# Kernel tuning notes

Hardware: AMD Instinct MI355X
Metric: run time of the kernel (lower is better)

Reference implementation:

```python
import jax, jax.numpy as jnp
import numpy as np

B, T, D = 2, 2048, 1024
H = 4            # num_heads (== num_kv_heads, num_kv_groups = 1)
W = 512          # window_size
S = 64           # state_size
CK = D // H      # head_k_dim = 256
CV = D // H      # head_v_dim = 256
EPS = 1e-5
SCALE = 1.0


def setup_inputs() -> dict:
    key = jax.random.key(0)
    ks = jax.random.split(key, 8)
    def w(k, o, i):
        return jax.random.normal(k, (o, i), jnp.float32) * 0.02
    return {
        "hidden_states": jax.random.normal(ks[0], (B, T, D), jnp.float32),
        "w_norm": jnp.ones((D,), jnp.float32),   # shared RMSNorm weight (pre- and post-norm; module overwrites self.norm)
        "Wq": w(ks[1], D, D),
        "Wk": w(ks[2], D, D),
        "Wv": w(ks[3], D, D),
        "Ws": w(ks[4], D, D),
        "Wg": w(ks[5], H * S, D),
        "Wo": w(ks[6], D, D),
    }


def _rms(x, w):
    return x * jax.lax.rsqrt(jnp.mean(x * x, axis=-1, keepdims=True) + EPS) * w


def reference(hidden_states, w_norm, Wq, Wk, Wv, Ws, Wg, Wo):
    h = _rms(hidden_states, w_norm)                           # pre-norm (norm_first)
    proj = lambda x, Wm: jnp.einsum('btd,od->bto', x, Wm)
    heads = lambda x, c: x.reshape(B, T, H, c).transpose(0, 2, 1, 3)
    q = heads(proj(h, Wq), CK) * SCALE                        # [B,H,T,CK]
    k = heads(proj(h, Wk), CK)
    v = heads(proj(h, Wv), CV)
    s = heads(proj(h, Ws), CK)                                # state-key projection
    g = jax.nn.softmax(proj(h, Wg), axis=-1)                  # softmax over full H*S dim (as in module)
    g = heads(g, S)                                           # [B,H,T,S] gate over state slots

    # ---- compressed global state (causal cumulative g-weighted outer products) ----
    # state_K[t] = sum_{t'<=t} g[t']^T s[t'];  scores_state[t,s] = q[t] . state_K[t,s]
    causal = jnp.tril(jnp.ones((T, T), dtype=bool))
    A = jnp.einsum('bhtc,bhuc->bhtu', q, s)                   # q . s per pair
    A = jnp.where(causal, A, 0.0)
    sc_state = jnp.einsum('bhtu,bhus->bhts', A, g)            # [B,H,T,S]

    # ---- sliding-window local attention (blocked: each query block sees prev+cur key block) ----
    nb = T // W
    qb = q.reshape(B, H, nb, W, CK)
    kb = k.reshape(B, H, nb, W, CK)
    vb = v.reshape(B, H, nb, W, CV)
    kprev = jnp.concatenate([jnp.zeros_like(kb[:, :, :1]), kb[:, :, :-1]], axis=2)
    vprev = jnp.concatenate([jnp.zeros_like(vb[:, :, :1]), vb[:, :, :-1]], axis=2)
    k2 = jnp.concatenate([kprev, kb], axis=3)                 # [B,H,nb,2W,CK]
    v2 = jnp.concatenate([vprev, vb], axis=3)                 # [B,H,nb,2W,CV]
    sc_w = jnp.einsum('bhnrc,bhnuc->bhnru', qb, k2)           # [B,H,nb,W,2W]

    r = jnp.arange(W)[:, None]
    u = jnp.arange(2 * W)[None, :]
    d = W + r - u                                             # distance t - t_key
    band = (d >= 0) & (d <= W - 1)                            # window of size W, causal
    first_blk = band & (u >= W)                               # block 0 has no real prev block
    wmask = jnp.where(jnp.arange(nb)[:, None, None] == 0, first_blk, band)   # [nb,W,2W]
    slopes = 2.0 ** (-8.0 * jnp.arange(H, dtype=jnp.float32) / H)            # [H]
    bias = -slopes[:, None, None] * d                          # alibi: slopes*(j-W+1) == -slope*dist
    sc_w = sc_w + bias[None, :, None, :, :]
    sc_w = jnp.where(wmask[None, None], sc_w, -1e30)

    # ---- joint softmax over [state ; window] columns ----
    sc = jnp.concatenate([sc_state.reshape(B, H, nb, W, S), sc_w], axis=-1)  # [B,H,nb,W,S+2W]
    p = jax.nn.softmax(sc, axis=-1)
    p_state = p[..., :S].reshape(B, H, T, S)
    p_w = p[..., S:]

    o_w = jnp.einsum('bhnru,bhnuc->bhnrc', p_w, v2).reshape(B, H, T, CV)
    # out_state[t] = sum_s p_state[t,s] * state_V[t,s],  state_V[t] = sum_{t'<=t} g[t']^T v[t']
    M = jnp.einsum('bhts,bhus->bhtu', p_state, g)
    M = jnp.where(causal, M, 0.0)
    o_s = jnp.einsum('bhtu,bhuc->bhtc', M, v)

    o = (o_w + o_s).transpose(0, 2, 1, 3).reshape(B, T, H * CV)
    o = o * jax.nn.sigmoid(o)                                  # swish
    o = _rms(o, w_norm)                                        # rms_norm_linear
    return jnp.einsum('btd,od->bto', o, Wo)
```

## Files before the change

kernel.cpp:

```cpp
#include <hip/hip_runtime.h>
#include <stdint.h>

#define B_  2
#define T_  2048
#define D_  1024
#define H_  4
#define S_  64
#define W_  512
#define CK_ 256
#define NC_ 32

typedef __attribute__((ext_vector_type(8))) short bf16x8;
typedef __attribute__((ext_vector_type(4))) float f32x4;
typedef __attribute__((ext_vector_type(4))) unsigned short u16x4;

__device__ __forceinline__ float bf2f(unsigned short u){ return __uint_as_float(((unsigned int)u)<<16); }
__device__ __forceinline__ unsigned short f2bf(float f){
  unsigned int u = __float_as_uint(f);
  u += 0x7fffu + ((u>>16)&1u);
  return (unsigned short)(u>>16);
}
__device__ __forceinline__ void split2(float y, unsigned short& hi, unsigned short& lo){
  hi = f2bf(y);
  lo = f2bf(y - bf2f(hi));
}

__device__ __forceinline__ void gl_lds16(const unsigned short* g, unsigned short* l){
  __builtin_amdgcn_global_load_lds(
      (const __attribute__((address_space(1))) unsigned int*)g,
      (__attribute__((address_space(3))) unsigned int*)l, 16, 0, 0);
}

__global__ void rmsnorm_split_kernel(const float* __restrict__ x, const float* __restrict__ w,
                                     unsigned short* __restrict__ ohi, unsigned short* __restrict__ olo){
  int row = blockIdx.x, tid = threadIdx.x;
  const float* xr = x + (size_t)row*D_;
  float v0=xr[tid], v1=xr[tid+256], v2=xr[tid+512], v3=xr[tid+768];
  __shared__ float red[256];
  red[tid] = v0*v0+v1*v1+v2*v2+v3*v3;
  __syncthreads();
  for(int s=128;s>0;s>>=1){ if(tid<s) red[tid]+=red[tid+s]; __syncthreads(); }
  float r = rsqrtf(red[0]/(float)D_ + 1e-5f);
  size_t base = (size_t)row*D_;
  float y0=v0*r*w[tid], y1=v1*r*w[tid+256], y2=v2*r*w[tid+512], y3=v3*r*w[tid+768];
  unsigned short hh, ll;
  split2(y0,hh,ll); ohi[base+tid]=hh;     olo[base+tid]=ll;
  split2(y1,hh,ll); ohi[base+tid+256]=hh; olo[base+tid+256]=ll;
  split2(y2,hh,ll); ohi[base+tid+512]=hh; olo[base+tid+512]=ll;
  split2(y3,hh,ll); ohi[base+tid+768]=hh; olo[base+tid+768]=ll;
}

__global__ void wsplit_kernel(const float* __restrict__ Wq, const float* __restrict__ Wk,
                              const float* __restrict__ Ws, const float* __restrict__ Wv,
                              const float* __restrict__ Wg, const float* __restrict__ Wo,
                              unsigned short* __restrict__ whi, unsigned short* __restrict__ wlo){
  int row = blockIdx.x, tid = threadIdx.x;
  const float* src;
  if(row < 1024)      src = Wq + (size_t)row*1024;
  else if(row < 2048) src = Wk + (size_t)(row-1024)*1024;
  else if(row < 3072) src = Ws + (size_t)(row-2048)*1024;
  else if(row < 4096) src = Wv + (size_t)(row-3072)*1024;
  else if(row < 4352) src = Wg + (size_t)(row-4096)*1024;
  else                src = Wo + (size_t)(row-4352)*1024;
  f32x4 vv = *(const f32x4*)(src + tid*4);
  u16x4 hh, ll;
  #pragma unroll
  for(int j=0;j<4;j++){ unsigned short a,b; split2(vv[j],a,b); hh[j]=a; ll[j]=b; }
  *(u16x4*)(whi + (size_t)row*1024 + tid*4) = hh;
  *(u16x4*)(wlo + (size_t)row*1024 + tid*4) = ll;
}

__global__ __launch_bounds__(256,2) void gemm_bf16s(
    const unsigned short* __restrict__ Ahi, const unsigned short* __restrict__ Alo,
    const unsigned short* __restrict__ Whi, const unsigned short* __restrict__ Wlo,
    unsigned short* __restrict__ qks, float* __restrict__ vout,
    unsigned short* __restrict__ vt, float* __restrict__ gout,
    float* __restrict__ Cf, int mode)
{
  __shared__ unsigned short Ah_s[128*64];
  __shared__ unsigned short Al_s[128*64];
  __shared__ unsigned short Bh_s[128*64];
  __shared__ unsigned short Bl_s[128*64];
  int tid = threadIdx.x;
  int lane = tid & 63, w = tid >> 6;
  int quad = lane >> 4, lq = lane & 15;
  int wr = w >> 1, wc = w & 1;
  int bid = blockIdx.y*gridDim.x + blockIdx.x;
  int row0, col0;
  if(mode == 0){
    int xcd = bid & 7, slot = bid >> 3;
    int rx = xcd & 3, cx = xcd >> 2;
    int sr = slot / 17, sc2 = slot % 17;
    row0 = (rx*8 + sr)*128;
    col0 = (cx*17 + sc2)*128;
  } else {
    int q8 = (gridDim.x*gridDim.y) >> 3;
    int wg = (bid & 7)*q8 + (bid >> 3);
    col0 = (wg % gridDim.x)*128;
    row0 = (wg / gridDim.x)*128;
  }

  int l8 = lane >> 3;
  int chk = lane & 7;

  f32x4 acc[4][4];
  #pragma unroll
  for(int i=0;i<4;i++)
    #pragma unroll
    for(int j=0;j<4;j++) acc[i][j] = (f32x4){0.f,0.f,0.f,0.f};

  for(int kt=0; kt<1024; kt+=64){
    __syncthreads();
    #pragma unroll
    for(int j=0;j<4;j++){
      int rl = w*32 + j*8 + l8;
      int sc = (chk ^ (rl & 7))*8;
      int lbase = (w*32 + j*8)*64;
      gl_lds16(Ahi + (size_t)(row0+rl)*1024 + kt + sc, Ah_s + lbase);
      gl_lds16(Alo + (size_t)(row0+rl)*1024 + kt + sc, Al_s + lbase);
      gl_lds16(Whi + (size_t)(col0+rl)*1024 + kt + sc, Bh_s + lbase);
      gl_lds16(Wlo + (size_t)(col0+rl)*1024 + kt + sc, Bl_s + lbase);
    }
    __syncthreads();
    #pragma unroll
    for(int ks=0;ks<2;ks++){
      bf16x8 afh[4], afl[4], bfh[4], bfl[4];
      #pragma unroll
      for(int i=0;i<4;i++){
        int Ra = wr*64+i*16+lq;
        int ca = ((ks*4+quad) ^ (Ra&7))*8;
        afh[i] = *(const bf16x8*)(const void*)(Ah_s + Ra*64 + ca);
        afl[i] = *(const bf16x8*)(const void*)(Al_s + Ra*64 + ca);
        int Rb = wc*64+i*16+lq;
        int cb = ((ks*4+quad) ^ (Rb&7))*8;
        bfh[i] = *(const bf16x8*)(const void*)(Bh_s + Rb*64 + cb);
        bfl[i] = *(const bf16x8*)(const void*)(Bl_s + Rb*64 + cb);
      }
      #pragma unroll
      for(int mi=0;mi<4;mi++)
        #pragma unroll
        for(int ni=0;ni<4;ni++){
          acc[mi][ni] = __builtin_amdgcn_mfma_f32_16x16x32_bf16(afh[mi], bfh[ni], acc[mi][ni], 0,0,0);
          acc[mi][ni] = __builtin_amdgcn_mfma_f32_16x16x32_bf16(afh[mi], bfl[ni], acc[mi][ni], 0,0,0);
          acc[mi][ni] = __builtin_amdgcn_mfma_f32_16x16x32_bf16(afl[mi], bfh[ni], acc[mi][ni], 0,0,0);
        }
    }
  }

  int rbase = row0 + wr*64, cbase = col0 + wc*64;
  if(mode == 1){
    #pragma unroll
    for(int mi=0;mi<4;mi++)
      #pragma unroll
      for(int ni=0;ni<4;ni++)
        #pragma unroll
        for(int i=0;i<4;i++)
          Cf[(size_t)(rbase+mi*16+quad*4+i)*1024 + cbase+ni*16+lq] = acc[mi][ni][i];
  } else if(col0 < 3072){
    unsigned short* dst = qks + (size_t)(col0>>10)*4194304;
    #pragma unroll
    for(int mi=0;mi<4;mi++)
      #pragma unroll
      for(int ni=0;ni<4;ni++)
        #pragma unroll
        for(int i=0;i<4;i++){
          int rr = rbase+mi*16+quad*4+i, cc = (cbase+ni*16+lq) & 1023;
          dst[(size_t)rr*1024 + cc] = f2bf(acc[mi][ni][i]);
        }
  } else if(col0 < 4096){
    #pragma unroll
    for(int mi=0;mi<4;mi++)
      #pragma unroll
      for(int ni=0;ni<4;ni++)
        #pragma unroll
        for(int i=0;i<4;i++){
          int rr = rbase+mi*16+quad*4+i, cl = (cbase+ni*16+lq) & 1023;
          float val = acc[mi][ni][i];
          vout[(size_t)rr*1024 + cl] = val;
          int hh = cl>>8, cv = cl&255, bb = rr>>11, tt = rr&2047;
          vt[((size_t)((bb*H_+hh)*256 + cv))*T_ + tt] = f2bf(val);
        }
  } else {
    #pragma unroll
    for(int mi=0;mi<4;mi++)
      #pragma unroll
      for(int ni=0;ni<4;ni++)
        #pragma unroll
        for(int i=0;i<4;i++){
          int rr = rbase+mi*16+quad*4+i, cl = cbase+ni*16+lq - 4096;
          gout[(size_t)rr*256 + cl] = acc[mi][ni][i];
        }
  }
}

__global__ void softmax256_kernel(float* __restrict__ g){
  int row = blockIdx.x, tid = threadIdx.x;
  float x = g[(size_t)row*256+tid];
  __shared__ float red[256];
  red[tid]=x; __syncthreads();
  for(int s=128;s>0;s>>=1){ if(tid<s) red[tid]=fmaxf(red[tid],red[tid+s]); __syncthreads(); }
  float m = red[0]; __syncthreads();
  float e = expf(x-m);
  red[tid]=e; __syncthreads();
  for(int s=128;s>0;s>>=1){ if(tid<s) red[tid]+=red[tid+s]; __syncthreads(); }
  g[(size_t)row*256+tid] = e/red[0];
}

__global__ __launch_bounds__(256,1) void chunk_outer_mfma(
    const unsigned short* __restrict__ gthi, const unsigned short* __restrict__ gtlo,
    const unsigned short* __restrict__ s_bf, const float* __restrict__ vf,
    float* __restrict__ out)
{
  __shared__ unsigned short xh_lds[256*72];
  __shared__ unsigned short xl_lds[256*72];
  int n=blockIdx.x, h=blockIdx.y, b=blockIdx.z;
  int tid=threadIdx.x, lane=tid&63, w=tid>>6;
  int quad=lane>>4, lq=lane&15;
  int t0=n*64, bh=b*H_+h;

  if(vf){
    const float* vb = vf + (size_t)(b*T_+t0)*D_ + h*CK_ + tid;
    for(int p2=0;p2<8;p2++){
      union{ unsigned short u[8]; bf16x8 v8; } hi8, lo8;
      #pragma unroll
      for(int j=0;j<8;j++)
        split2(vb[(size_t)(p2*8+j)*D_], hi8.u[j], lo8.u[j]);
      *(bf16x8*)(void*)&xh_lds[tid*72 + p2*8] = hi8.v8;
      *(bf16x8*)(void*)&xl_lds[tid*72 + p2*8] = lo8.v8;
    }
  } else {
    const unsigned short* sb = s_bf + (size_t)(b*T_+t0)*D_ + h*CK_ + tid;
    for(int p2=0;p2<8;p2++){
      union{ unsigned short u[8]; bf16x8 v8; } r8;
      #pragma unroll
      for(int j=0;j<8;j++)
        r8.u[j] = sb[(size_t)(p2*8+j)*D_];
      *(bf16x8*)(void*)&xh_lds[tid*72 + p2*8] = r8.v8;
    }
  }
  __syncthreads();

  size_t gtbase = ((size_t)bh*NC_ + n)*64;
  f32x4 acc[4][4];
  #pragma unroll
  for(int i=0;i<4;i++)
    #pragma unroll
    for(int j=0;j<4;j++) acc[i][j] = (f32x4){0.f,0.f,0.f,0.f};

  #pragma unroll
  for(int ks=0; ks<2; ks++){
    bf16x8 ah[4], al[4], bh4[4], bl4[4];
    #pragma unroll
    for(int mi=0;mi<4;mi++){
      ah[mi] = *(const bf16x8*)(const void*)(gthi + (gtbase + mi*16+lq)*64 + ks*32 + quad*8);
      al[mi] = *(const bf16x8*)(const void*)(gtlo + (gtbase + mi*16+lq)*64 + ks*32 + quad*8);
    }
    #pragma unroll
    for(int ni=0;ni<4;ni++){
      bh4[ni] = *(const bf16x8*)(const void*)&xh_lds[(w*64+ni*16+lq)*72 + ks*32 + quad*8];
      if(vf) bl4[ni] = *(const bf16x8*)(const void*)&xl_lds[(w*64+ni*16+lq)*72 + ks*32 + quad*8];
    }
    #pragma unroll
    for(int mi=0;mi<4;mi++)
      #pragma unroll
      for(int ni=0;ni<4;ni++){
        acc[mi][ni] = __builtin_amdgcn_mfma_f32_16x16x32_bf16(ah[mi], bh4[ni], acc[mi][ni], 0,0,0);
        acc[mi][ni] = __builtin_amdgcn_mfma_f32_16x16x32_bf16(al[mi], bh4[ni], acc[mi][ni], 0,0,0);
        if(vf) acc[mi][ni] = __builtin_amdgcn_mfma_f32_16x16x32_bf16(ah[mi], bl4[ni], acc[mi][ni], 0,0,0);
      }
  }
  size_t obase = ((size_t)bh*NC_ + n)*16384;
  #pragma unroll
  for(int mi=0;mi<4;mi++)
    #pragma unroll
    for(int ni=0;ni<4;ni++)
      #pragma unroll
      for(int i=0;i<4;i++){
        int s = mi*16 + quad*4 + i, c = w*64 + ni*16 + lq;
        out[obase + (size_t)s*256 + c] = acc[mi][ni][i];
      }
}

__global__ void chunk_prefix_kernel(float* __restrict__ arr){
  int idx = blockIdx.x*256 + threadIdx.x;
  int bh = idx >> 14, e = idx & 16383;
  float run = 0.f;
  size_t base = (size_t)bh*NC_*16384 + e;
  for(int n=0;n<NC_;n++){
    size_t a = base + (size_t)n*16384;
    float t = arr[a]; arr[a] = run; run += t;
  }
}

__global__ void chunk_prefix_split_kernel(const float* __restrict__ arr,
    unsigned short* __restrict__ hi, unsigned short* __restrict__ lo){
  int idx = blockIdx.x*256 + threadIdx.x;
  int bh = idx >> 14, e = idx & 16383;
  float run = 0.f;
  size_t base = (size_t)bh*NC_*16384 + e;
  for(int n=0;n<NC_;n++){
    size_t a = base + (size_t)n*16384;
    float t = arr[a];
    unsigned short hh, ll;
    split2(run, hh, ll);
    hi[a] = hh; lo[a] = ll;
    run += t;
  }
}

__global__ __launch_bounds__(256) void g_transpose_split_kernel(const float* __restrict__ g,
    unsigned short* __restrict__ gthi, unsigned short* __restrict__ gtlo){
  int n=blockIdx.x, h=blockIdx.y, b=blockIdx.z;
  int tid=threadIdx.x, t0=n*64;
  __shared__ float tt[64][65];
  #pragma unroll
  for(int p=0;p<16;p++){
    int u = (tid>>6) + p*4, s = tid&63;
    tt[s][u] = g[((size_t)(b*T_ + t0 + u))*256 + h*64 + s];
  }
  __syncthreads();
  size_t base = ((size_t)(b*H_+h)*NC_ + n)*64;
  #pragma unroll
  for(int p=0;p<16;p++){
    int s = (tid>>6) + p*4, u = tid&63;
    unsigned short hh, ll;
    split2(tt[s][u], hh, ll);
    gthi[(base+s)*64 + u] = hh;
    gtlo[(base+s)*64 + u] = ll;
  }
}

__global__ __launch_bounds__(256,1) void sc_state_mfma(
    const unsigned short* __restrict__ q_bf,
    const unsigned short* __restrict__ s_bf,
    const unsigned short* __restrict__ S1hi, const unsigned short* __restrict__ S1lo,
    const unsigned short* __restrict__ gthi, const unsigned short* __restrict__ gtlo,
    float* __restrict__ sc_state)
{
  int n=blockIdx.x, h=blockIdx.y, b=blockIdx.z;
  int tid=threadIdx.x, lane=tid&63, w=tid>>6;
  int quad=lane>>4, lq=lane&15;
  int t0=n*64, bh=b*H_+h, strip=w*16;

  __shared__ unsigned short A_hi[64*72];
  __shared__ unsigned short A_lo[64*72];

  bf16x8 qf[8];
  const unsigned short* qrow = q_bf + ((size_t)(b*T_ + t0 + strip + lq))*D_ + h*CK_ + quad*8;
  #pragma unroll
  for(int ks=0;ks<8;ks++) qf[ks] = *(const bf16x8*)(const void*)(qrow + ks*32);

  const unsigned short* sbase = s_bf + ((size_t)(b*T_ + t0))*D_ + h*CK_;
  f32x4 a1[4];
  #pragma unroll
  for(int nf=0;nf<4;nf++) a1[nf] = (f32x4){0.f,0.f,0.f,0.f};
  #pragma unroll
  for(int ks=0;ks<8;ks++){
    #pragma unroll
    for(int nf=0;nf<4;nf++){
      bf16x8 sf = *(const bf16x8*)(const void*)(sbase + (size_t)(nf*16+lq)*D_ + ks*32 + quad*8);
      a1[nf] = __builtin_amdgcn_mfma_f32_16x16x32_bf16(qf[ks], sf, a1[nf], 0,0,0);
    }
  }
  #pragma unroll
  for(int nf=0;nf<4;nf++){
    int u = nf*16 + lq;
    #pragma unroll
    for(int i=0;i<4;i++){
      int trow = strip + quad*4 + i;
      float val = (u <= trow) ? a1[nf][i] : 0.f;
      unsigned short hh, ll;
      split2(val, hh, ll);
      A_hi[trow*72 + u] = hh;
      A_lo[trow*72 + u] = ll;
    }
  }
  __syncthreads();

  bf16x8 afh[2], afl[2];
  #pragma unroll
  for(int ks=0;ks<2;ks++){
    afh[ks] = *(const bf16x8*)(const void*)&A_hi[(strip+lq)*72 + ks*32 + quad*8];
    afl[ks] = *(const bf16x8*)(const void*)&A_lo[(strip+lq)*72 + ks*32 + quad*8];
  }

  size_t s1base = ((size_t)bh*NC_ + n)*16384;
  size_t gtbase = ((size_t)bh*NC_ + n)*64;
  f32x4 acc2[4];
  #pragma unroll
  for(int nf=0;nf<4;nf++) acc2[nf] = (f32x4){0.f,0.f,0.f,0.f};
  #pragma unroll
  for(int ks=0;ks<8;ks++){
    #pragma unroll
    for(int nf=0;nf<4;nf++){
      size_t off = s1base + (size_t)(nf*16+lq)*256 + ks*32 + quad*8;
      bf16x8 b1 = *(const bf16x8*)(const void*)(S1hi + off);
      acc2[nf] = __builtin_amdgcn_mfma_f32_16x16x32_bf16(qf[ks], b1, acc2[nf], 0,0,0);
      bf16x8 b2 = *(const bf16x8*)(const void*)(S1lo + off);
      acc2[nf] = __builtin_amdgcn_mfma_f32_16x16x32_bf16(qf[ks], b2, acc2[nf], 0,0,0);
    }
  }
  #pragma unroll
  for(int ks=0;ks<2;ks++){
    #pragma unroll
    for(int nf=0;nf<4;nf++){
      size_t off = (gtbase + nf*16+lq)*64 + ks*32 + quad*8;
      bf16x8 gh = *(const bf16x8*)(const void*)(gthi + off);
      bf16x8 gl = *(const bf16x8*)(const void*)(gtlo + off);
      acc2[nf] = __builtin_amdgcn_mfma_f32_16x16x32_bf16(afh[ks], gh, acc2[nf], 0,0,0);
      acc2[nf] = __builtin_amdgcn_mfma_f32_16x16x32_bf16(afh[ks], gl, acc2[nf], 0,0,0);
      acc2[nf] = __builtin_amdgcn_mfma_f32_16x16x32_bf16(afl[ks], gh, acc2[nf], 0,0,0);
    }
  }
  #pragma unroll
  for(int nf=0;nf<4;nf++){
    #pragma unroll
    for(int i=0;i<4;i++){
      int trow = strip + quad*4 + i;
      sc_state[((size_t)bh*T_ + t0 + trow)*64 + nf*16+lq] = acc2[nf][i];
    }
  }
}

__global__ __launch_bounds__(256,1) void window_attn_mfma(
    const unsigned short* __restrict__ q_bf,
    const unsigned short* __restrict__ k_bf,
    const unsigned short* __restrict__ vt_bf,
    const float* __restrict__ sc_state,
    float* __restrict__ o, float* __restrict__ p_state)
{
  int nt=blockIdx.x, h=blockIdx.y, b=blockIdx.z;
  int tid=threadIdx.x;
  int lane = tid & 63, w = tid >> 6;
  int quad = lane >> 4, lq = lane & 15;
  int sp = w >> 1, np = w & 1;
  int t0 = nt*64, bh = b*H_ + h;
  float slope = exp2f(-2.0f*(float)h);

  __shared__ unsigned short kv_lds[256*72];
  __shared__ float S_lds[64*68];
  __shared__ unsigned short P_lds[64*72];
  __shared__ float m_lds[64], l_lds[64], al_lds[64];

  bf16x8 qf[2][8];
  #pragma unroll
  for(int st=0; st<2; st++){
    const unsigned short* qrow = q_bf + ((size_t)(b*T_ + t0 + 32*sp + 16*st + lq))*D_ + h*CK_ + quad*8;
    #pragma unroll
    for(int ks=0; ks<8; ks++)
      qf[st][ks] = *(const bf16x8*)(const void*)(qrow + ks*32);
  }

  int r = tid >> 2, part = tid & 3;
  {
    const float* scrow = sc_state + ((size_t)bh*T_ + t0 + r)*64 + part*16;
    float pm = -1e30f, sv[16];
    #pragma unroll
    for(int i=0;i<16;i++){ sv[i] = scrow[i]; pm = fmaxf(pm, sv[i]); }
    pm = fmaxf(pm, __shfl_xor(pm,1)); pm = fmaxf(pm, __shfl_xor(pm,2));
    float ps = 0.f;
    #pragma unroll
    for(int i=0;i<16;i++) ps += __expf(sv[i]-pm);
    ps += __shfl_xor(ps,1); ps += __shfl_xor(ps,2);
    if(part==0){ m_lds[r]=pm; l_lds[r]=ps; }
  }

  f32x4 o_acc[2][8];
  #pragma unroll
  for(int st=0;st<2;st++)
    #pragma unroll
    for(int nv=0;nv<8;nv++) o_acc[st][nv] = (f32x4){0.f,0.f,0.f,0.f};
  __syncthreads();

  int jt0 = (nt>=8)? nt-8 : 0;
  for(int jt=jt0; jt<=nt; jt++){
    int j0 = jt*64;
    {
      int row = tid>>2, seg = tid&3;
      const unsigned short* src = k_bf + ((size_t)(b*T_ + j0 + row))*D_ + h*CK_ + seg*64;
      unsigned short* dst = kv_lds + row*260 + seg*64;
      #pragma unroll
      for(int i=0;i<8;i++) *(bf16x8*)(void*)(dst + i*8) = *(const bf16x8*)(const void*)(src + i*8);
    }
    __syncthreads();
    f32x4 sacc[2][2];
    #pragma unroll
    for(int st=0;st<2;st++)
      #pragma unroll
      for(int n2=0;n2<2;n2++) sacc[st][n2] = (f32x4){0.f,0.f,0.f,0.f};
    #pragma unroll
    for(int n2=0;n2<2;n2++){
      int n = np*2 + n2;
      #pragma unroll
      for(int ks=0;ks<8;ks++){
        bf16x8 kf = *(const bf16x8*)(const void*)(kv_lds + (n*16+lq)*260 + ks*32 + quad*8);
        sacc[0][n2] = __builtin_amdgcn_mfma_f32_16x16x32_bf16(qf[0][ks], kf, sacc[0][n2], 0,0,0);
        sacc[1][n2] = __builtin_amdgcn_mfma_f32_16x16x32_bf16(qf[1][ks], kf, sacc[1][n2], 0,0,0);
      }
    }
    #pragma unroll
    for(int st=0;st<2;st++){
      #pragma unroll
      for(int n2=0;n2<2;n2++){
        int n = np*2+n2;
        int u = j0 + n*16 + lq;
        #pragma unroll
        for(int i=0;i<4;i++){
          int row = 32*sp + 16*st + quad*4 + i;
          int d = (t0 + row) - u;
          float val = (d>=0 && d<W_) ? sacc[st][n2][i] - slope*(float)d : -1e30f;
          S_lds[row*68 + n*16+lq] = val;
        }
      }
    }
    __syncthreads();
    {
      float s16[16], tm = -1e30f;
      #pragma unroll
      for(int i=0;i<16;i++){ s16[i] = S_lds[r*68 + part*16 + i]; tm = fmaxf(tm, s16[i]); }
      tm = fmaxf(tm, __shfl_xor(tm,1)); tm = fmaxf(tm, __shfl_xor(tm,2));
      float m_old = m_lds[r];
      float m_new = fmaxf(m_old, tm);
      float alpha = __expf(m_old - m_new);
      float ts = 0.f;
      union { unsigned short u[16]; bf16x8 v[2]; } pk;
      #pragma unroll
      for(int i=0;i<16;i++){ float p = __expf(s16[i]-m_new); ts += p; pk.u[i] = f2bf(p); }
      ts += __shfl_xor(ts,1); ts += __shfl_xor(ts,2);
      *(bf16x8*)(void*)&P_lds[r*72 + part*16]     = pk.v[0];
      *(bf16x8*)(void*)&P_lds[r*72 + part*16 + 8] = pk.v[1];
      if(part==0){ m_lds[r] = m_new; l_lds[r] = l_lds[r]*alpha + ts; al_lds[r] = alpha; }
      #pragma unroll
      for(int pass=0; pass<4; pass++){
        int cv = (tid>>2) + 64*pass, useg = (tid&3)*16;
        const unsigned short* src = vt_bf + ((size_t)(bh*256 + cv))*T_ + j0 + useg;
        unsigned short* dst = kv_lds + cv*72 + useg;
        *(bf16x8*)(void*)(dst)   = *(const bf16x8*)(const void*)(src);
        *(bf16x8*)(void*)(dst+8) = *(const bf16x8*)(const void*)(src+8);
      }
    }
    __syncthreads();
    #pragma unroll
    for(int st=0;st<2;st++){
      #pragma unroll
      for(int i=0;i<4;i++){
        float al = al_lds[32*sp+16*st+quad*4+i];
        #pragma unroll
        for(int nv=0;nv<8;nv++) o_acc[st][nv][i] *= al;
      }
    }
    bf16x8 pa[2][2];
    #pragma unroll
    for(int st=0;st<2;st++)
      #pragma unroll
      for(int k2=0;k2<2;k2++)
        pa[st][k2] = *(const bf16x8*)(const void*)&P_lds[(32*sp+16*st+lq)*72 + k2*32 + quad*8];
    #pragma unroll
    for(int nv=0;nv<8;nv++){
      int cvt = np*8 + nv;
      #pragma unroll
      for(int k2=0;k2<2;k2++){
        bf16x8 vb = *(const bf16x8*)(const void*)(kv_lds + (cvt*16+lq)*72 + k2*32 + quad*8);
        o_acc[0][nv] = __builtin_amdgcn_mfma_f32_16x16x32_bf16(pa[0][k2], vb, o_acc[0][nv], 0,0,0);
        o_acc[1][nv] = __builtin_amdgcn_mfma_f32_16x16x32_bf16(pa[1][k2], vb, o_acc[1][nv], 0,0,0);
      }
    }
    __syncthreads();
  }
  #pragma unroll
  for(int st=0;st<2;st++){
    #pragma unroll
    for(int i=0;i<4;i++){
      int row = 32*sp+16*st+quad*4+i;
      float rl = 1.0f / l_lds[row];
      #pragma unroll
      for(int nv=0;nv<8;nv++){
        int cv = (np*8+nv)*16 + lq;
        o[((size_t)bh*T_ + t0 + row)*256 + cv] = o_acc[st][nv][i] * rl;
      }
    }
  }
  {
    float mf = m_lds[r], rlf = 1.0f / l_lds[r];
    const float* scrow = sc_state + ((size_t)bh*T_ + t0 + r)*64 + part*16;
    float* pr = p_state + ((size_t)bh*T_ + t0 + r)*64 + part*16;
    #pragma unroll
    for(int i=0;i<16;i++) pr[i] = __expf(scrow[i]-mf)*rlf;
  }
}

__global__ __launch_bounds__(256) void o_state_kernel(const float* __restrict__ p_state,
    const float* __restrict__ g,
    const float* __restrict__ v, const float* __restrict__ SG, float* __restrict__ o){
  int n=blockIdx.x, h=blockIdx.y, b=blockIdx.z;
  int tid=threadIdx.x, t0=n*64;
  __shared__ float p_lds[64*69];
  __shared__ float g_lds[64*69];
  __shared__ float M_lds[64*65];
  for(int i=0;i<16;i++){
    int rr = (tid>>6) + i*4, cc = tid&63;
    p_lds[rr*69+cc] = p_state[((size_t)(b*H_+h)*T_ + t0+rr)*64 + cc];
    g_lds[rr*69+cc] = g[((size_t)(b*T_+t0+rr))*256 + h*64 + cc];
  }
  __syncthreads();
  int u = tid & 63;
  #pragma unroll 1
  for(int kk=0;kk<16;kk++){
    int t = (tid>>6) + kk*4;
    float dot=0.f;
    #pragma unroll
    for(int s=0;s<64;s++) dot += p_lds[t*69+s]*g_lds[u*69+s];
    M_lds[t*65+u] = (u<=t)? dot : 0.f;
  }
  __syncthreads();
  float acc[64];
  #pragma unroll
  for(int t=0;t<64;t++) acc[t]=0.f;
  size_t sgbase = ((size_t)(b*H_+h)*NC_+n)*16384;
  for(int s=0;s<64;s++){
    float gsc = SG[sgbase + s*256 + tid];
    #pragma unroll
    for(int t=0;t<64;t++) acc[t] += p_lds[t*69+s]*gsc;
  }
  for(int uu=0;uu<64;uu++){
    float vv = v[((size_t)(b*T_+t0+uu))*D_ + h*CK_ + tid];
    #pragma unroll
    for(int t=0;t<64;t++) acc[t] += M_lds[t*65+uu]*vv;
  }
  #pragma unroll 4
  for(int t=0;t<64;t++){
    size_t oi = ((size_t)(b*H_+h)*T_ + t0+t)*256 + tid;
    o[oi] += acc[t];
  }
}

__global__ void swish_rms_split_kernel(const float* __restrict__ o, const float* __restrict__ w,
                                       unsigned short* __restrict__ ohi, unsigned short* __restrict__ olo){
  int bt=blockIdx.x, tid=threadIdx.x;
  int b = bt >> 11, t = bt & 2047;
  float y[4]; float ss=0.f;
  #pragma unroll
  for(int hh=0;hh<4;hh++){
    float x = o[((size_t)(b*H_+hh)*T_ + t)*256 + tid];
    float yy = x / (1.f + expf(-x));
    y[hh]=yy; ss += yy*yy;
  }
  __shared__ float red[256];
  red[tid]=ss; __syncthreads();
  for(int s2=128;s2>0;s2>>=1){ if(tid<s2) red[tid]+=red[tid+s2]; __syncthreads(); }
  float r = rsqrtf(red[0]/1024.f + 1e-5f);
  #pragma unroll
  for(int hh=0;hh<4;hh++){
    unsigned short a,bq;
    split2(y[hh]*r*w[hh*256+tid], a, bq);
    ohi[(size_t)bt*1024 + hh*256 + tid] = a;
    olo[(size_t)bt*1024 + hh*256 + tid] = bq;
  }
}

extern "C" void kernel_launch(void* const* d_in, const int* in_sizes, int n_in,
                              void* d_out, int out_size, void* d_ws, size_t ws_size,
                              hipStream_t stream){
  const float* hidden = (const float*)d_in[0];
  const float* w_norm = (const float*)d_in[1];
  const float* Wq = (const float*)d_in[2];
  const float* Wk = (const float*)d_in[3];
  const float* Wv = (const float*)d_in[4];
  const float* Ws = (const float*)d_in[5];
  const float* Wg = (const float*)d_in[6];
  const float* Wo = (const float*)d_in[7];
  float* out = (float*)d_out;

  char* p = (char*)d_ws;
  auto alloc = [&](size_t bytes)->void*{ void* r = (void*)p; p += (bytes + 255) & ~(size_t)255; return r; };
  unsigned short* h_hi = (unsigned short*)alloc(8388608);
  unsigned short* h_lo = (unsigned short*)alloc(8388608);
  unsigned short* Wc_hi = (unsigned short*)alloc(11010048);
  unsigned short* Wc_lo = (unsigned short*)alloc(11010048);
  float* v   = (float*)alloc(16777216);
  float* g   = (float*)alloc(4194304);
  float* P1  = (float*)alloc(16777216);
  float* P2  = (float*)alloc(16777216);
  float* sc  = (float*)alloc(4194304);
  float* ps  = (float*)alloc(4194304);
  unsigned short* qks = (unsigned short*)alloc(25165824);
  unsigned short* vt  = (unsigned short*)alloc(8388608);

  unsigned short* q_bf = qks;
  unsigned short* k_bf = qks + 4194304;
  unsigned short* s_bf = qks + 8388608;
  float* o = P1;
  unsigned short* S1hi = (unsigned short*)P2;
  unsigned short* S1lo = S1hi + 4194304;
  unsigned short* GThi = (unsigned short*)ps;
  unsigned short* GTlo = GThi + 1048576;

  rmsnorm_split_kernel<<<4096,256,0,stream>>>(hidden, w_norm, h_hi, h_lo);
  wsplit_kernel<<<5376,256,0,stream>>>(Wq, Wk, Ws, Wv, Wg, Wo, Wc_hi, Wc_lo);
  gemm_bf16s<<<dim3(34,32),256,0,stream>>>(h_hi, h_lo, Wc_hi, Wc_lo,
                                           qks, v, vt, g, nullptr, 0);
  softmax256_kernel<<<4096,256,0,stream>>>(g);
  dim3 gc(32,4,2);
  g_transpose_split_kernel<<<gc,256,0,stream>>>(g, GThi, GTlo);
  chunk_outer_mfma<<<gc,256,0,stream>>>(GThi, GTlo, s_bf, nullptr, P1);
  chunk_prefix_split_kernel<<<512,256,0,stream>>>(P1, S1hi, S1lo);
  sc_state_mfma<<<gc,256,0,stream>>>(q_bf, s_bf, S1hi, S1lo, GThi, GTlo, sc);
  chunk_outer_mfma<<<gc,256,0,stream>>>(GThi, GTlo, nullptr, v, P2);
  chunk_prefix_kernel<<<512,256,0,stream>>>(P2);
  window_attn_mfma<<<gc,256,0,stream>>>(q_bf, k_bf, vt, sc, o, ps);
  o_state_kernel<<<gc,256,0,stream>>>(ps, g, v, P2, o);
  swish_rms_split_kernel<<<4096,256,0,stream>>>(o, w_norm, h_hi, h_lo);
  gemm_bf16s<<<dim3(8,32),256,0,stream>>>(h_hi, h_lo, Wc_hi + (size_t)4352*1024, Wc_lo + (size_t)4352*1024,
                                          nullptr, nullptr, nullptr, nullptr, out, 1);
}
```

Baseline: 463.7 us.

## Move state-output computation to split-bf16 MFMA and store v only as transposed hi/lo

Replaces the scalar fp32 o_state kernel, which does three 64-deep FMA loops per thread, with an MFMA kernel. It builds the causal p·gᵀ matrix with split-bf16 MFMAs in LDS, then accumulates p·S2 and M·v with hi/lo MFMA triples. The GEMM epilogue now writes v only as transposed hi/lo bf16 instead of fp32 plus bf16. The v-state chunk outer product reads this transposed v directly and writes its output transposed, so the prefix-split kernel can produce the bf16 hi/lo state. The point is to remove slow scalar FP32 work and strided fp32 v loads, at the cost of extra split/convert work, buffer aliasing and split-bf16 precision error.

```diff
diff --git a/kernel.cpp b/kernel.cpp
--- a/kernel.cpp
+++ b/kernel.cpp
@@ -73,8 +73,8 @@
 __global__ __launch_bounds__(256,2) void gemm_bf16s(
     const unsigned short* __restrict__ Ahi, const unsigned short* __restrict__ Alo,
     const unsigned short* __restrict__ Whi, const unsigned short* __restrict__ Wlo,
-    unsigned short* __restrict__ qks, float* __restrict__ vout,
-    unsigned short* __restrict__ vt, float* __restrict__ gout,
+    unsigned short* __restrict__ qks, unsigned short* __restrict__ vt,
+    unsigned short* __restrict__ vtlo, float* __restrict__ gout,
     float* __restrict__ Cf, int mode)
 {
   __shared__ unsigned short Ah_s[128*64];
@@ -175,10 +175,12 @@
         #pragma unroll
         for(int i=0;i<4;i++){
           int rr = rbase+mi*16+quad*4+i, cl = (cbase+ni*16+lq) & 1023;
-          float val = acc[mi][ni][i];
-          vout[(size_t)rr*1024 + cl] = val;
+          unsigned short hh2, ll2;
+          split2(acc[mi][ni][i], hh2, ll2);
           int hh = cl>>8, cv = cl&255, bb = rr>>11, tt = rr&2047;
-          vt[((size_t)((bb*H_+hh)*256 + cv))*T_ + tt] = f2bf(val);
+          size_t ti = ((size_t)((bb*H_+hh)*256 + cv))*T_ + tt;
+          vt[ti] = hh2;
+          vtlo[ti] = ll2;
         }
   } else {
     #pragma unroll
@@ -208,35 +210,21 @@
 
 __global__ __launch_bounds__(256,1) void chunk_outer_mfma(
     const unsigned short* __restrict__ gthi, const unsigned short* __restrict__ gtlo,
-    const unsigned short* __restrict__ s_bf, const float* __restrict__ vf,
-    float* __restrict__ out)
+    const unsigned short* __restrict__ s_bf, float* __restrict__ out)
 {
   __shared__ unsigned short xh_lds[256*72];
-  __shared__ unsigned short xl_lds[256*72];
   int n=blockIdx.x, h=blockIdx.y, b=blockIdx.z;
   int tid=threadIdx.x, lane=tid&63, w=tid>>6;
   int quad=lane>>4, lq=lane&15;
   int t0=n*64, bh=b*H_+h;
 
-  if(vf){
-    const float* vb = vf + (size_t)(b*T_+t0)*D_ + h*CK_ + tid;
-    for(int p2=0;p2<8;p2++){
-      union{ unsigned short u[8]; bf16x8 v8; } hi8, lo8;
-      #pragma unroll
-      for(int j=0;j<8;j++)
-        split2(vb[(size_t)(p2*8+j)*D_], hi8.u[j], lo8.u[j]);
-      *(bf16x8*)(void*)&xh_lds[tid*72 + p2*8] = hi8.v8;
-      *(bf16x8*)(void*)&xl_lds[tid*72 + p2*8] = lo8.v8;
-    }
-  } else {
-    const unsigned short* sb = s_bf + (size_t)(b*T_+t0)*D_ + h*CK_ + tid;
-    for(int p2=0;p2<8;p2++){
-      union{ unsigned short u[8]; bf16x8 v8; } r8;
-      #pragma unroll
-      for(int j=0;j<8;j++)
-        r8.u[j] = sb[(size_t)(p2*8+j)*D_];
-      *(bf16x8*)(void*)&xh_lds[tid*72 + p2*8] = r8.v8;
-    }
+  const unsigned short* sb = s_bf + (size_t)(b*T_+t0)*D_ + h*CK_ + tid;
+  for(int p2=0;p2<8;p2++){
+    union{ unsigned short u[8]; bf16x8 v8; } r8;
+    #pragma unroll
+    for(int j=0;j<8;j++)
+      r8.u[j] = sb[(size_t)(p2*8+j)*D_];
+    *(bf16x8*)(void*)&xh_lds[tid*72 + p2*8] = r8.v8;
   }
   __syncthreads();
 
@@ -249,24 +237,21 @@
 
   #pragma unroll
   for(int ks=0; ks<2; ks++){
-    bf16x8 ah[4], al[4], bh4[4], bl4[4];
+    bf16x8 ah[4], al[4], bh4[4];
     #pragma unroll
     for(int mi=0;mi<4;mi++){
       ah[mi] = *(const bf16x8*)(const void*)(gthi + (gtbase + mi*16+lq)*64 + ks*32 + quad*8);
       al[mi] = *(const bf16x8*)(const void*)(gtlo + (gtbase + mi*16+lq)*64 + ks*32 + quad*8);
     }
     #pragma unroll
-    for(int ni=0;ni<4;ni++){
+    for(int ni=0;ni<4;ni++)
       bh4[ni] = *(const bf16x8*)(const void*)&xh_lds[(w*64+ni*16+lq)*72 + ks*32 + quad*8];
-      if(vf) bl4[ni] = *(const bf16x8*)(const void*)&xl_lds[(w*64+ni*16+lq)*72 + ks*32 + quad*8];
-    }
     #pragma unroll
     for(int mi=0;mi<4;mi++)
       #pragma unroll
       for(int ni=0;ni<4;ni++){
         acc[mi][ni] = __builtin_amdgcn_mfma_f32_16x16x32_bf16(ah[mi], bh4[ni], acc[mi][ni], 0,0,0);
         acc[mi][ni] = __builtin_amdgcn_mfma_f32_16x16x32_bf16(al[mi], bh4[ni], acc[mi][ni], 0,0,0);
-        if(vf) acc[mi][ni] = __builtin_amdgcn_mfma_f32_16x16x32_bf16(ah[mi], bl4[ni], acc[mi][ni], 0,0,0);
       }
   }
   size_t obase = ((size_t)bh*NC_ + n)*16384;
@@ -281,15 +266,51 @@
       }
 }
 
-__global__ void chunk_prefix_kernel(float* __restrict__ arr){
-  int idx = blockIdx.x*256 + threadIdx.x;
-  int bh = idx >> 14, e = idx & 16383;
-  float run = 0.f;
-  size_t base = (size_t)bh*NC_*16384 + e;
-  for(int n=0;n<NC_;n++){
-    size_t a = base + (size_t)n*16384;
-    float t = arr[a]; arr[a] = run; run += t;
-  }
+__global__ __launch_bounds__(256,1) void chunk_outer_vt(
+    const unsigned short* __restrict__ gthi, const unsigned short* __restrict__ gtlo,
+    const unsigned short* __restrict__ vt, const unsigned short* __restrict__ vtlo,
+    float* __restrict__ out)
+{
+  int n=blockIdx.x, h=blockIdx.y, b=blockIdx.z;
+  int tid=threadIdx.x, lane=tid&63, w=tid>>6;
+  int quad=lane>>4, lq=lane&15;
+  int t0=n*64, bh=b*H_+h;
+  size_t gtbase = ((size_t)bh*NC_ + n)*64;
+  f32x4 acc[4][4];
+  #pragma unroll
+  for(int i=0;i<4;i++)
+    #pragma unroll
+    for(int j=0;j<4;j++) acc[i][j] = (f32x4){0.f,0.f,0.f,0.f};
+
+  #pragma unroll
+  for(int ks=0; ks<2; ks++){
+    bf16x8 ah[4], al[4];
+    #pragma unroll
+    for(int mi=0;mi<4;mi++){
+      ah[mi] = *(const bf16x8*)(const void*)(gthi + (gtbase + mi*16+lq)*64 + ks*32 + quad*8);
+      al[mi] = *(const bf16x8*)(const void*)(gtlo + (gtbase + mi*16+lq)*64 + ks*32 + quad*8);
+    }
+    #pragma unroll
+    for(int ni=0;ni<4;ni++){
+      size_t vo = ((size_t)(bh*256 + w*64 + ni*16 + lq))*T_ + t0 + ks*32 + quad*8;
+      bf16x8 vh = *(const bf16x8*)(const void*)(vt + vo);
+      bf16x8 vl = *(const bf16x8*)(const void*)(vtlo + vo);
+      #pragma unroll
+      for(int mi=0;mi<4;mi++){
+        acc[mi][ni] = __builtin_amdgcn_mfma_f32_16x16x32_bf16(ah[mi], vh, acc[mi][ni], 0,0,0);
+        acc[mi][ni] = __builtin_amdgcn_mfma_f32_16x16x32_bf16(al[mi], vh, acc[mi][ni], 0,0,0);
+        acc[mi][ni] = __builtin_amdgcn_mfma_f32_16x16x32_bf16(ah[mi], vl, acc[mi][ni], 0,0,0);
+      }
+    }
+  }
+  size_t obase = ((size_t)bh*NC_ + n)*16384;
+  #pragma unroll
+  for(int mi=0;mi<4;mi++)
+    #pragma unroll
+    for(int ni=0;ni<4;ni++){
+      int c = w*64 + ni*16 + lq, s0 = mi*16 + quad*4;
+      *(f32x4*)&out[obase + (size_t)c*64 + s0] = acc[mi][ni];
+    }
 }
 
 __global__ void chunk_prefix_split_kernel(const float* __restrict__ arr,
@@ -427,7 +448,8 @@
     const unsigned short* __restrict__ k_bf,
     const unsigned short* __restrict__ vt_bf,
     const float* __restrict__ sc_state,
-    float* __restrict__ o, float* __restrict__ p_state)
+    float* __restrict__ o,
+    unsigned short* __restrict__ phi, unsigned short* __restrict__ plo)
 {
   int nt=blockIdx.x, h=blockIdx.y, b=blockIdx.z;
   int tid=threadIdx.x;
@@ -583,55 +605,130 @@
   {
     float mf = m_lds[r], rlf = 1.0f / l_lds[r];
     const float* scrow = sc_state + ((size_t)bh*T_ + t0 + r)*64 + part*16;
-    float* pr = p_state + ((size_t)bh*T_ + t0 + r)*64 + part*16;
-    #pragma unroll
-    for(int i=0;i<16;i++) pr[i] = __expf(scrow[i]-mf)*rlf;
-  }
-}
-
-__global__ __launch_bounds__(256) void o_state_kernel(const float* __restrict__ p_state,
+    size_t pb = ((size_t)bh*T_ + t0 + r)*64 + part*16;
+    #pragma unroll
+    for(int i=0;i<16;i++){
+      float pv = __expf(scrow[i]-mf)*rlf;
+      unsigned short hh, ll;
+      split2(pv, hh, ll);
+      phi[pb+i] = hh;
+      plo[pb+i] = ll;
+    }
+  }
+}
+
+__global__ __launch_bounds__(256,1) void o_state_mfma(
+    const unsigned short* __restrict__ phi, const unsigned short* __restrict__ plo,
     const float* __restrict__ g,
-    const float* __restrict__ v, const float* __restrict__ SG, float* __restrict__ o){
+    const unsigned short* __restrict__ S2hi, const unsigned short* __restrict__ S2lo,
+    const unsigned short* __restrict__ vt, const unsigned short* __restrict__ vtlo,
+    float* __restrict__ o)
+{
+  __shared__ unsigned short gh_lds[64*72];
+  __shared__ unsigned short gl_lds[64*72];
+  __shared__ unsigned short Mh_lds[64*72];
+  __shared__ unsigned short Ml_lds[64*72];
   int n=blockIdx.x, h=blockIdx.y, b=blockIdx.z;
-  int tid=threadIdx.x, t0=n*64;
-  __shared__ float p_lds[64*69];
-  __shared__ float g_lds[64*69];
-  __shared__ float M_lds[64*65];
-  for(int i=0;i<16;i++){
-    int rr = (tid>>6) + i*4, cc = tid&63;
-    p_lds[rr*69+cc] = p_state[((size_t)(b*H_+h)*T_ + t0+rr)*64 + cc];
-    g_lds[rr*69+cc] = g[((size_t)(b*T_+t0+rr))*256 + h*64 + cc];
+  int tid=threadIdx.x, lane=tid&63, w=tid>>6;
+  int quad=lane>>4, lq=lane&15;
+  int t0=n*64, bh=b*H_+h, strip=w*16;
+
+  {
+    int gu = tid>>2, gs0 = (tid&3)*16;
+    const float* gr = g + ((size_t)(b*T_+t0+gu))*256 + h*64 + gs0;
+    union{ unsigned short u[16]; bf16x8 v[2]; } GH, GL;
+    #pragma unroll
+    for(int j=0;j<16;j++) split2(gr[j], GH.u[j], GL.u[j]);
+    *(bf16x8*)(void*)&gh_lds[gu*72+gs0]   = GH.v[0];
+    *(bf16x8*)(void*)&gh_lds[gu*72+gs0+8] = GH.v[1];
+    *(bf16x8*)(void*)&gl_lds[gu*72+gs0]   = GL.v[0];
+    *(bf16x8*)(void*)&gl_lds[gu*72+gs0+8] = GL.v[1];
   }
   __syncthreads();
-  int u = tid & 63;
-  #pragma unroll 1
-  for(int kk=0;kk<16;kk++){
-    int t = (tid>>6) + kk*4;
-    float dot=0.f;
-    #pragma unroll
-    for(int s=0;s<64;s++) dot += p_lds[t*69+s]*g_lds[u*69+s];
-    M_lds[t*65+u] = (u<=t)? dot : 0.f;
+
+  {
+    const unsigned short* ph = phi + ((size_t)bh*T_ + t0 + strip + lq)*64;
+    const unsigned short* pl = plo + ((size_t)bh*T_ + t0 + strip + lq)*64;
+    f32x4 ma[4];
+    #pragma unroll
+    for(int nf=0;nf<4;nf++) ma[nf] = (f32x4){0.f,0.f,0.f,0.f};
+    #pragma unroll
+    for(int ks=0;ks<2;ks++){
+      bf16x8 pfh = *(const bf16x8*)(const void*)(ph + ks*32 + quad*8);
+      bf16x8 pfl = *(const bf16x8*)(const void*)(pl + ks*32 + quad*8);
+      #pragma unroll
+      for(int nf=0;nf<4;nf++){
+        bf16x8 gH = *(const bf16x8*)(const void*)&gh_lds[(nf*16+lq)*72 + ks*32 + quad*8];
+        bf16x8 gL = *(const bf16x8*)(const void*)&gl_lds[(nf*16+lq)*72 + ks*32 + quad*8];
+        ma[nf] = __builtin_amdgcn_mfma_f32_16x16x32_bf16(pfh, gH, ma[nf], 0,0,0);
+        ma[nf] = __builtin_amdgcn_mfma_f32_16x16x32_bf16(pfh, gL, ma[nf], 0,0,0);
+        ma[nf] = __builtin_amdgcn_mfma_f32_16x16x32_bf16(pfl, gH, ma[nf], 0,0,0);
+      }
+    }
+    #pragma unroll
+    for(int nf=0;nf<4;nf++){
+      int u = nf*16 + lq;
+      #pragma unroll
+      for(int i=0;i<4;i++){
+        int trow = strip + quad*4 + i;
+        float val = (u <= trow) ? ma[nf][i] : 0.f;
+        unsigned short hh, ll;
+        split2(val, hh, ll);
+        Mh_lds[trow*72 + u] = hh;
+        Ml_lds[trow*72 + u] = ll;
+      }
+    }
   }
   __syncthreads();
-  float acc[64];
-  #pragma unroll
-  for(int t=0;t<64;t++) acc[t]=0.f;
-  size_t sgbase = ((size_t)(b*H_+h)*NC_+n)*16384;
-  for(int s=0;s<64;s++){
-    float gsc = SG[sgbase + s*256 + tid];
-    #pragma unroll
-    for(int t=0;t<64;t++) acc[t] += p_lds[t*69+s]*gsc;
-  }
-  for(int uu=0;uu<64;uu++){
-    float vv = v[((size_t)(b*T_+t0+uu))*D_ + h*CK_ + tid];
-    #pragma unroll
-    for(int t=0;t<64;t++) acc[t] += M_lds[t*65+uu]*vv;
-  }
-  #pragma unroll 4
-  for(int t=0;t<64;t++){
-    size_t oi = ((size_t)(b*H_+h)*T_ + t0+t)*256 + tid;
-    o[oi] += acc[t];
-  }
+
+  f32x4 oacc[4][4];
+  #pragma unroll
+  for(int i=0;i<4;i++)
+    #pragma unroll
+    for(int j=0;j<4;j++) oacc[i][j] = (f32x4){0.f,0.f,0.f,0.f};
+  int c0 = w*64;
+  size_t sgbase = ((size_t)bh*NC_ + n)*16384;
+  #pragma unroll
+  for(int ks=0;ks<2;ks++){
+    bf16x8 pAh[4], pAl[4], mAh[4], mAl[4];
+    #pragma unroll
+    for(int mi=0;mi<4;mi++){
+      size_t po = ((size_t)bh*T_ + t0 + mi*16+lq)*64 + ks*32 + quad*8;
+      pAh[mi] = *(const bf16x8*)(const void*)(phi + po);
+      pAl[mi] = *(const bf16x8*)(const void*)(plo + po);
+      mAh[mi] = *(const bf16x8*)(const void*)&Mh_lds[(mi*16+lq)*72 + ks*32 + quad*8];
+      mAl[mi] = *(const bf16x8*)(const void*)&Ml_lds[(mi*16+lq)*72 + ks*32 + quad*8];
+    }
+    #pragma unroll
+    for(int ni=0;ni<4;ni++){
+      int c = c0 + ni*16 + lq;
+      size_t so = sgbase + (size_t)c*64 + ks*32 + quad*8;
+      bf16x8 sgH = *(const bf16x8*)(const void*)(S2hi + so);
+      bf16x8 sgL = *(const bf16x8*)(const void*)(S2lo + so);
+      size_t vo = ((size_t)(bh*256 + c))*T_ + t0 + ks*32 + quad*8;
+      bf16x8 vH = *(const bf16x8*)(const void*)(vt + vo);
+      bf16x8 vL = *(const bf16x8*)(const void*)(vtlo + vo);
+      #pragma unroll
+      for(int mi=0;mi<4;mi++){
+        oacc[mi][ni] = __builtin_amdgcn_mfma_f32_16x16x32_bf16(pAh[mi], sgH, oacc[mi][ni], 0,0,0);
+        oacc[mi][ni] = __builtin_amdgcn_mfma_f32_16x16x32_bf16(pAh[mi], sgL, oacc[mi][ni], 0,0,0);
+        oacc[mi][ni] = __builtin_amdgcn_mfma_f32_16x16x32_bf16(pAl[mi], sgH, oacc[mi][ni], 0,0,0);
+        oacc[mi][ni] = __builtin_amdgcn_mfma_f32_16x16x32_bf16(mAh[mi], vH, oacc[mi][ni], 0,0,0);
+        oacc[mi][ni] = __builtin_amdgcn_mfma_f32_16x16x32_bf16(mAl[mi], vH, oacc[mi][ni], 0,0,0);
+        oacc[mi][ni] = __builtin_amdgcn_mfma_f32_16x16x32_bf16(mAh[mi], vL, oacc[mi][ni], 0,0,0);
+      }
+    }
+  }
+  #pragma unroll
+  for(int mi=0;mi<4;mi++)
+    #pragma unroll
+    for(int ni=0;ni<4;ni++)
+      #pragma unroll
+      for(int i=0;i<4;i++){
+        int trow = mi*16 + quad*4 + i, c = c0 + ni*16 + lq;
+        size_t oi = ((size_t)bh*T_ + t0 + trow)*256 + c;
+        o[oi] += oacc[mi][ni][i];
+      }
 }
 
 __global__ void swish_rms_split_kernel(const float* __restrict__ o, const float* __restrict__ w,
@@ -677,7 +774,7 @@
   unsigned short* h_lo = (unsigned short*)alloc(8388608);
   unsigned short* Wc_hi = (unsigned short*)alloc(11010048);
   unsigned short* Wc_lo = (unsigned short*)alloc(11010048);
-  float* v   = (float*)alloc(16777216);
+  unsigned short* vslot = (unsigned short*)alloc(16777216);
   float* g   = (float*)alloc(4194304);
   float* P1  = (float*)alloc(16777216);
   float* P2  = (float*)alloc(16777216);
@@ -686,29 +783,34 @@
   unsigned short* qks = (unsigned short*)alloc(25165824);
   unsigned short* vt  = (unsigned short*)alloc(8388608);
 
+  unsigned short* vtlo = vslot;
+  unsigned short* S2hi = vslot + 4194304;
   unsigned short* q_bf = qks;
   unsigned short* k_bf = qks + 4194304;
   unsigned short* s_bf = qks + 8388608;
+  unsigned short* S2lo = s_bf;
   float* o = P1;
   unsigned short* S1hi = (unsigned short*)P2;
   unsigned short* S1lo = S1hi + 4194304;
   unsigned short* GThi = (unsigned short*)ps;
   unsigned short* GTlo = GThi + 1048576;
+  unsigned short* phi  = (unsigned short*)ps;
+  unsigned short* plo  = phi + 1048576;
 
   rmsnorm_split_kernel<<<4096,256,0,stream>>>(hidden, w_norm, h_hi, h_lo);
   wsplit_kernel<<<5376,256,0,stream>>>(Wq, Wk, Ws, Wv, Wg, Wo, Wc_hi, Wc_lo);
   gemm_bf16s<<<dim3(34,32),256,0,stream>>>(h_hi, h_lo, Wc_hi, Wc_lo,
-                                           qks, v, vt, g, nullptr, 0);
+                                           qks, vt, vtlo, g, nullptr, 0);
   softmax256_kernel<<<4096,256,0,stream>>>(g);
   dim3 gc(32,4,2);
   g_transpose_split_kernel<<<gc,256,0,stream>>>(g, GThi, GTlo);
-  chunk_outer_mfma<<<gc,256,0,stream>>>(GThi, GTlo, s_bf, nullptr, P1);
+  chunk_outer_mfma<<<gc,256,0,stream>>>(GThi, GTlo, s_bf, P1);
   chunk_prefix_split_kernel<<<512,256,0,stream>>>(P1, S1hi, S1lo);
   sc_state_mfma<<<gc,256,0,stream>>>(q_bf, s_bf, S1hi, S1lo, GThi, GTlo, sc);
-  chunk_outer_mfma<<<gc,256,0,stream>>>(GThi, GTlo, nullptr, v, P2);
-  chunk_prefix_kernel<<<512,256,0,stream>>>(P2);
-  window_attn_mfma<<<gc,256,0,stream>>>(q_bf, k_bf, vt, sc, o, ps);
-  o_state_kernel<<<gc,256,0,stream>>>(ps, g, v, P2, o);
+  chunk_outer_vt<<<gc,256,0,stream>>>(GThi, GTlo, vt, vtlo, P2);
+  chunk_prefix_split_kernel<<<512,256,0,stream>>>(P2, S2hi, S2lo);
+  window_attn_mfma<<<gc,256,0,stream>>>(q_bf, k_bf, vt, sc, o, phi, plo);
+  o_state_mfma<<<gc,256,0,stream>>>(phi, plo, g, S2hi, S2lo, vt, vtlo, o);
   swish_rms_split_kernel<<<4096,256,0,stream>>>(o, w_norm, h_hi, h_lo);
   gemm_bf16s<<<dim3(8,32),256,0,stream>>>(h_hi, h_lo, Wc_hi + (size_t)4352*1024, Wc_lo + (size_t)4352*1024,
                                           nullptr, nullptr, nullptr, nullptr, out, 1);
```

After: 385.5 us. -16.9%, faster.
